# Performance work log

Measured on AMD Instinct MI355X. Metric: run time of the kernel, lower is better.

## Reference

```python
import jax, jax.numpy as jnp
import numpy as np
from jax import lax

NPOINT = 1024
RADIUS = 0.2
NSAMPLE = 32
BN_EPS = 1e-5


def square_distance(src, dst):
    # src: [B,N,3], dst: [B,M,3] -> [B,N,M]
    d = -2.0 * jnp.einsum('bnc,bmc->bnm', src, dst)
    d = d + jnp.sum(src * src, -1)[:, :, None]
    d = d + jnp.sum(dst * dst, -1)[:, None, :]
    return d


def farthest_point_sample(xyz, npoint):
    # Deterministic start at index 0 (torch version uses a random start).
    B, N, _ = xyz.shape
    batch = jnp.arange(B)

    def step(carry, _):
        distance, farthest = carry
        centroid = xyz[batch, farthest][:, None, :]          # [B,1,3]
        dist = jnp.sum((xyz - centroid) ** 2, -1)            # [B,N]
        distance = jnp.minimum(distance, dist)
        new_far = jnp.argmax(distance, -1).astype(jnp.int32)
        return (distance, new_far), farthest

    init = (jnp.full((B, N), 1e10, xyz.dtype), jnp.zeros((B,), jnp.int32))
    _, cents = lax.scan(step, init, None, length=npoint)     # [npoint,B]
    return cents.T                                           # [B,npoint]


def index_points(points, idx):
    # points: [B,N,C], idx: [B,...] -> [B,...,C]
    return jax.vmap(lambda p, i: p[i])(points, idx)


def query_ball_point(radius, nsample, xyz, new_xyz):
    B, N, _ = xyz.shape
    sqr = square_distance(new_xyz, xyz)                      # [B,S,N]
    gidx = jnp.where(sqr > radius * radius, N,
                     jnp.arange(N, dtype=jnp.int32)[None, None, :])
    gidx = jnp.sort(gidx, axis=-1)[:, :, :nsample]           # [B,S,nsample]
    first = gidx[:, :, :1]
    return jnp.where(gidx == N, first, gidx)


def conv_bn_relu(x, w, b, g, beta):
    # x: [B,Cin,K,S]; 1x1 conv + training-mode BN + ReLU
    y = jnp.einsum('bcks,oc->boks', x, w) + b[None, :, None, None]
    mean = jnp.mean(y, axis=(0, 2, 3), keepdims=True)
    var = jnp.var(y, axis=(0, 2, 3), keepdims=True)
    y = (y - mean) * lax.rsqrt(var + BN_EPS)
    y = y * g[None, :, None, None] + beta[None, :, None, None]
    return jax.nn.relu(y)


def setup_inputs() -> dict:
    key = jax.random.key(0)
    ks = jax.random.split(key, 8)
    B, N, D = 16, 4096, 64
    inp = {
        'xyz': jax.random.uniform(ks[0], (B, N, 3), jnp.float32),
        'points': jax.random.normal(ks[1], (B, N, D), jnp.float32),
        'w1': jax.random.normal(ks[2], (64, 67), jnp.float32) * 0.1,
        'b1': jax.random.normal(ks[3], (64,), jnp.float32) * 0.1,
        'g1': jnp.ones((64,), jnp.float32),
        'beta1': jnp.zeros((64,), jnp.float32),
        'w2': jax.random.normal(ks[4], (64, 64), jnp.float32) * 0.1,
        'b2': jax.random.normal(ks[5], (64,), jnp.float32) * 0.1,
        'g2': jnp.ones((64,), jnp.float32),
        'beta2': jnp.zeros((64,), jnp.float32),
        'w3': jax.random.normal(ks[6], (128, 64), jnp.float32) * 0.1,
        'b3': jax.random.normal(ks[7], (128,), jnp.float32) * 0.1,
        'g3': jnp.ones((128,), jnp.float32),
        'beta3': jnp.zeros((128,), jnp.float32),
    }
    return inp


def reference(xyz, points, w1, b1, g1, beta1, w2, b2, g2, beta2, w3, b3, g3, beta3):
    B, N, C = xyz.shape
    fps_idx = farthest_point_sample(xyz, NPOINT)                 # [B,S]
    new_xyz = index_points(xyz, fps_idx)                         # [B,S,3]
    idx = query_ball_point(RADIUS, NSAMPLE, xyz, new_xyz)        # [B,S,K]
    grouped_xyz = index_points(xyz, idx) - new_xyz[:, :, None, :]  # [B,S,K,3]
    grouped_points = jnp.concatenate([grouped_xyz, index_points(points, idx)], axis=-1)  # [B,S,K,3+D]
    x = jnp.transpose(grouped_points, (0, 3, 2, 1))              # [B,C,K,S]
    x = conv_bn_relu(x, w1, b1, g1, beta1)
    x = conv_bn_relu(x, w2, b2, g2, beta2)
    x = conv_bn_relu(x, w3, b3, g3, beta3)
    new_points = jnp.max(x, axis=2)                              # [B,C_out,S]
    new_points = jnp.transpose(new_points, (0, 2, 1))            # [B,S,C_out]
    return (new_xyz, new_points)
```

## Files before the change

kernel.cpp:

```cpp
#include <hip/hip_runtime.h>
#include <stdint.h>

#define NPOINT 1024
#define NSAMPLE 32
#define NB 16
#define NN 4096
#define BN_EPS 1e-5
#define NPIX (NB*NPOINT*NSAMPLE)
#define NBLK 8192

__device__ __forceinline__ float sqdist3(float dx, float dy, float dz) {
  #pragma clang fp contract(off)
  float a = dx*dx; float b = dy*dy; float c = dz*dz;
  return (a + b) + c;
}

#define FPS_T 512
#define FPS_PTS (NN/FPS_T)
#define FPS_W (FPS_T/64)

#define DPP_MAX64V(VAR, CTRL)                                                  \
  {                                                                            \
    long long kl = __double_as_longlong(VAR);                                  \
    int lo = (int)(unsigned int)kl, hi = (int)(kl >> 32);                      \
    int olo = __builtin_amdgcn_update_dpp(lo, lo, (CTRL), 0xf, 0xf, false);    \
    int ohi = __builtin_amdgcn_update_dpp(hi, hi, (CTRL), 0xf, 0xf, false);    \
    double ok = __longlong_as_double(((long long)ohi << 32) |                  \
                                     (unsigned long long)(unsigned int)olo);   \
    VAR = fmax(VAR, ok);                                                       \
  }

__global__ __launch_bounds__(512) void fps_kernel(
    const float* __restrict__ xyz, int* __restrict__ cents_g) {
  __shared__ __align__(16) float4 pos[NN];
  __shared__ __align__(16) double keybuf[2][FPS_W];
  __shared__ int cents_l[NPOINT];
  const int b = blockIdx.x;
  const int t = threadIdx.x;
  const float* base = xyz + (size_t)b * NN * 3;
  for (int i = t; i < NN; i += FPS_T) {
    pos[i] = make_float4(base[3*i+0], base[3*i+1], base[3*i+2], 0.f);
  }
  __syncthreads();
  float px[FPS_PTS], py[FPS_PTS], pz[FPS_PTS], dist[FPS_PTS];
  int lowj[FPS_PTS];
  #pragma unroll
  for (int i = 0; i < FPS_PTS; i++) {
    float4 p = pos[i*FPS_T + t];
    px[i] = p.x; py[i] = p.y; pz[i] = p.z;
    dist[i] = 1e10f;
    lowj[i] = (NN-1) - (i*FPS_T + t);
  }
  const int lane = t & 63, wid = t >> 6;
  int far = 0;
  for (int it = 0; it < NPOINT; it++) {
    if (t == 0) cents_l[it] = far;
    float4 c = pos[far];
    float nd[FPS_PTS];
    #pragma unroll
    for (int i = 0; i < FPS_PTS; i++) {
      float d = sqdist3(px[i]-c.x, py[i]-c.y, pz[i]-c.z);
      nd[i] = fminf(dist[i], d);
      dist[i] = nd[i];
    }
    double kk[FPS_PTS];
    #pragma unroll
    for (int i = 0; i < FPS_PTS; i++) {
      kk[i] = __longlong_as_double(
          ((long long)__float_as_int(nd[i]) << 32) |
          (unsigned long long)(unsigned int)lowj[i]);
    }
    double bk = fmax(fmax(fmax(kk[0], kk[1]), fmax(kk[2], kk[3])),
                     fmax(fmax(kk[4], kk[5]), fmax(kk[6], kk[7])));
    DPP_MAX64V(bk, 0x111);
    DPP_MAX64V(bk, 0x112);
    DPP_MAX64V(bk, 0x114);
    DPP_MAX64V(bk, 0x118);
    DPP_MAX64V(bk, 0x142);
    DPP_MAX64V(bk, 0x143);
    const int p = it & 1;
    if (lane == 63) keybuf[p][wid] = bk;
    __syncthreads();
    double k = keybuf[p][lane & (FPS_W-1)];
    DPP_MAX64V(k, 0x111);
    DPP_MAX64V(k, 0x112);
    DPP_MAX64V(k, 0x114);
    int lo32 = (int)(unsigned int)__double_as_longlong(k);
    far = (NN-1) - __builtin_amdgcn_readlane(lo32, 7);
  }
  __syncthreads();
  for (int i = t; i < NPOINT; i += FPS_T) cents_g[b*NPOINT + i] = cents_l[i];
}

__global__ __launch_bounds__(256) void ballquery_kernel(
    const float* __restrict__ xyz, const int* __restrict__ cents_g,
    int* __restrict__ idx) {
  const int w = blockIdx.x * 4 + (threadIdx.x >> 6);
  const int lane = threadIdx.x & 63;
  const int b = w >> 10;
  const double RR = 0.2 * 0.2;
  const int cj = cents_g[w] & (NN-1);
  const float* cptr = xyz + ((size_t)b * NN + cj) * 3;
  const double cx = (double)cptr[0], cy = (double)cptr[1], cz = (double)cptr[2];
  const double cn = cx*cx + cy*cy + cz*cz;
  const float* base = xyz + (size_t)b * NN * 3;
  int* out = idx + (size_t)w * NSAMPLE;
  int have = 0, firstj = 0;
  for (int j0 = 0; j0 < NN; j0 += 64) {
    int j = j0 + lane;
    double x = (double)base[3*j+0];
    double y = (double)base[3*j+1];
    double z = (double)base[3*j+2];
    double pn = x*x + y*y + z*z;
    double d = -2.0*(cx*x + cy*y + cz*z) + cn + pn;
    bool pass = !(d > RR);
    unsigned long long m = __ballot(pass);
    int cnt = __popcll(m);
    if (have == 0 && cnt > 0) firstj = j0 + (__ffsll((unsigned long long)m) - 1);
    if (pass) {
      int pos = have + __popcll(m & ((1ull << lane) - 1ull));
      if (pos < NSAMPLE) out[pos] = j;
    }
    have += cnt;
    if (have >= NSAMPLE) break;
  }
  for (int k = have + lane; k < NSAMPLE; k += 64) out[k] = firstj;
}

template<int MODE, bool STOREY>
__global__ __launch_bounds__(256) void fused_pass(
    const float* __restrict__ xyz, const float* __restrict__ points,
    const int* __restrict__ cents_g, const int* __restrict__ idx,
    const float* __restrict__ w1, const float* __restrict__ b1,
    const float* __restrict__ w2, const float* __restrict__ b2,
    const float* __restrict__ w3, const float* __restrict__ b3,
    const double* __restrict__ aff1, const double* __restrict__ aff2,
    double* __restrict__ partial, float* __restrict__ pmax, float* __restrict__ pmin,
    float* __restrict__ ystore) {
  __shared__ float wbuf[67*64];
  __shared__ float xsm[67*68];
  __shared__ float bsm[64];
  __shared__ float bsm2[64];
  __shared__ float sc1m[64], sh1m[64], sc2m[64], sh2m[64];
  const int t = threadIdx.x;
  const int pb = blockIdx.x * 64;
  const int tr = t & 15, tc = t >> 4;
  double* pout = partial + (size_t)blockIdx.x * 256;

  for (int ii = t; ii < 67*64; ii += 256) {
    int oc = ii & 63, cc = ii >> 6;
    wbuf[cc*64 + oc] = w1[oc*67 + cc];
  }
  if (t < 64) {
    bsm[t] = b1[t];
    if (MODE >= 2) { sc1m[t] = (float)aff1[t]; sh1m[t] = (float)aff1[128+t]; }
    if (MODE >= 3) { sc2m[t] = (float)aff2[t]; sh2m[t] = (float)aff2[128+t]; }
  }
  {
    const int pxl = t >> 2, q = t & 3;
    const int p = pb + pxl;
    const int bs = p >> 5;
    const int b  = p >> 15;
    const int j  = idx[p] & (NN-1);
    const float4* prow = (const float4*)(points + ((size_t)b * NN + j) * 64);
    #pragma unroll
    for (int u = 0; u < 4; u++) {
      float4 v = prow[q*4 + u];
      int c0 = 3 + q*16 + u*4;
      xsm[(c0+0)*68 + pxl] = v.x;
      xsm[(c0+1)*68 + pxl] = v.y;
      xsm[(c0+2)*68 + pxl] = v.z;
      xsm[(c0+3)*68 + pxl] = v.w;
    }
    if (q == 0) {
      const float* xr = xyz + ((size_t)b * NN + j) * 3;
      const int cj = cents_g[bs] & (NN-1);
      const float* ce = xyz + ((size_t)b * NN + cj) * 3;
      xsm[0*68 + pxl] = xr[0] - ce[0];
      xsm[1*68 + pxl] = xr[1] - ce[1];
      xsm[2*68 + pxl] = xr[2] - ce[2];
    }
  }
  __syncthreads();

  float acc[4][4] = {};
  for (int cc = 0; cc < 67; cc++) {
    float4 xv = *(const float4*)&xsm[cc*68 + 4*tr];
    float4 wv = *(const float4*)&wbuf[cc*64 + 4*tc];
    float xa[4] = {xv.x, xv.y, xv.z, xv.w};
    float wa[4] = {wv.x, wv.y, wv.z, wv.w};
    #pragma unroll
    for (int i = 0; i < 4; i++)
      #pragma unroll
      for (int jj = 0; jj < 4; jj++) acc[i][jj] += xa[i]*wa[jj];
  }
  if constexpr (MODE == 1) {
    if constexpr (STOREY) {
      #pragma unroll
      for (int i = 0; i < 4; i++) {
        float4 o = make_float4(acc[i][0], acc[i][1], acc[i][2], acc[i][3]);
        *(float4*)(ystore + ((size_t)(pb + 4*tr + i))*64 + 4*tc) = o;
      }
    }
    double s1[4] = {0,0,0,0}, s2[4] = {0,0,0,0};
    #pragma unroll
    for (int jj = 0; jj < 4; jj++) {
      float bb = bsm[4*tc+jj];
      #pragma unroll
      for (int i = 0; i < 4; i++) {
        double yd = (double)(acc[i][jj] + bb);
        s1[jj] += yd; s2[jj] += yd*yd;
      }
    }
    #pragma unroll
    for (int off = 8; off > 0; off >>= 1)
      #pragma unroll
      for (int jj = 0; jj < 4; jj++) {
        s1[jj] += __shfl_down(s1[jj], off, 16);
        s2[jj] += __shfl_down(s2[jj], off, 16);
      }
    if (tr == 0)
      #pragma unroll
      for (int jj = 0; jj < 4; jj++) {
        pout[4*tc+jj]       = s1[jj];
        pout[128 + 4*tc+jj] = s2[jj];
      }
    return;
  }

  __syncthreads();
  #pragma unroll
  for (int jj = 0; jj < 4; jj++) {
    int oc = 4*tc + jj;
    float bb = bsm[oc], sc = sc1m[oc], sh = sh1m[oc];
    float r[4];
    #pragma unroll
    for (int i = 0; i < 4; i++) r[i] = fmaxf((acc[i][jj] + bb)*sc + sh, 0.f);
    *(float4*)&xsm[oc*68 + 4*tr] = make_float4(r[0], r[1], r[2], r[3]);
  }
  for (int ii = t; ii < 4096; ii += 256) {
    int oc = ii & 63, cc = ii >> 6;
    wbuf[cc*64 + oc] = w2[oc*64 + cc];
  }
  if (t < 64) bsm2[t] = b2[t];
  __syncthreads();

  float acc2[4][4] = {};
  for (int cc = 0; cc < 64; cc++) {
    float4 xv = *(const float4*)&xsm[cc*68 + 4*tr];
    float4 wv = *(const float4*)&wbuf[cc*64 + 4*tc];
    float xa[4] = {xv.x, xv.y, xv.z, xv.w};
    float wa[4] = {wv.x, wv.y, wv.z, wv.w};
    #pragma unroll
    for (int i = 0; i < 4; i++)
      #pragma unroll
      for (int jj = 0; jj < 4; jj++) acc2[i][jj] += xa[i]*wa[jj];
  }
  if constexpr (MODE == 2) {
    if constexpr (STOREY) {
      #pragma unroll
      for (int i = 0; i < 4; i++) {
        float4 o = make_float4(acc2[i][0], acc2[i][1], acc2[i][2], acc2[i][3]);
        *(float4*)(ystore + ((size_t)(pb + 4*tr + i))*64 + 4*tc) = o;
      }
    }
    double s1[4] = {0,0,0,0}, s2[4] = {0,0,0,0};
    #pragma unroll
    for (int jj = 0; jj < 4; jj++) {
      float bb = bsm2[4*tc+jj];
      #pragma unroll
      for (int i = 0; i < 4; i++) {
        double yd = (double)(acc2[i][jj] + bb);
        s1[jj] += yd; s2[jj] += yd*yd;
      }
    }
    #pragma unroll
    for (int off = 8; off > 0; off >>= 1)
      #pragma unroll
      for (int jj = 0; jj < 4; jj++) {
        s1[jj] += __shfl_down(s1[jj], off, 16);
        s2[jj] += __shfl_down(s2[jj], off, 16);
      }
    if (tr == 0)
      #pragma unroll
      for (int jj = 0; jj < 4; jj++) {
        pout[4*tc+jj]       = s1[jj];
        pout[128 + 4*tc+jj] = s2[jj];
      }
    return;
  }

  if constexpr (MODE == 3) {
    __syncthreads();
    #pragma unroll
    for (int jj = 0; jj < 4; jj++) {
      int oc = 4*tc + jj;
      float bb = bsm2[oc], sc = sc2m[oc], sh = sh2m[oc];
      float r[4];
      #pragma unroll
      for (int i = 0; i < 4; i++) r[i] = fmaxf((acc2[i][jj] + bb)*sc + sh, 0.f);
      *(float4*)&xsm[oc*68 + 4*tr] = make_float4(r[0], r[1], r[2], r[3]);
    }
    for (int h = 0; h < 2; h++) {
      for (int ii = t; ii < 4096; ii += 256) {
        int oc = ii & 63, cc = ii >> 6;
        wbuf[cc*64 + oc] = w3[(h*64 + oc)*64 + cc];
      }
      if (t < 64) bsm[t] = b3[h*64 + t];
      __syncthreads();
      float acc3[4][4] = {};
      for (int cc = 0; cc < 64; cc++) {
        float4 xv = *(const float4*)&xsm[cc*68 + 4*tr];
        float4 wv = *(const float4*)&wbuf[cc*64 + 4*tc];
        float xa[4] = {xv.x, xv.y, xv.z, xv.w};
        float wa[4] = {wv.x, wv.y, wv.z, wv.w};
        #pragma unroll
        for (int i = 0; i < 4; i++)
          #pragma unroll
          for (int jj = 0; jj < 4; jj++) acc3[i][jj] += xa[i]*wa[jj];
      }
      double s1[4] = {0,0,0,0}, s2[4] = {0,0,0,0};
      float pmx[4], pmn[4];
      #pragma unroll
      for (int jj = 0; jj < 4; jj++) { pmx[jj] = -3.4e38f; pmn[jj] = 3.4e38f; }
      #pragma unroll
      for (int jj = 0; jj < 4; jj++) {
        float bb = bsm[4*tc+jj];
        #pragma unroll
        for (int i = 0; i < 4; i++) {
          float y = acc3[i][jj] + bb;
          double yd = (double)y;
          s1[jj] += yd; s2[jj] += yd*yd;
          pmx[jj] = fmaxf(pmx[jj], y); pmn[jj] = fminf(pmn[jj], y);
        }
      }
      #pragma unroll
      for (int off = 8; off > 0; off >>= 1)
        #pragma unroll
        for (int jj = 0; jj < 4; jj++) {
          s1[jj] += __shfl_down(s1[jj], off, 16);
          s2[jj] += __shfl_down(s2[jj], off, 16);
        }
      if (tr == 0)
        #pragma unroll
        for (int jj = 0; jj < 4; jj++) {
          pout[h*64 + 4*tc+jj]       = s1[jj];
          pout[128 + h*64 + 4*tc+jj] = s2[jj];
        }
      #pragma unroll
      for (int off = 4; off > 0; off >>= 1)
        #pragma unroll
        for (int jj = 0; jj < 4; jj++) {
          pmx[jj] = fmaxf(pmx[jj], __shfl_down(pmx[jj], off, 8));
          pmn[jj] = fminf(pmn[jj], __shfl_down(pmn[jj], off, 8));
        }
      if ((tr & 7) == 0) {
        int bs = (pb >> 5) + (tr >> 3);
        size_t ob = (size_t)bs*128 + h*64 + 4*tc;
        #pragma unroll
        for (int jj = 0; jj < 4; jj++) {
          pmax[ob + jj] = pmx[jj];
          pmin[ob + jj] = pmn[jj];
        }
      }
      __syncthreads();
    }
  }
}

__global__ __launch_bounds__(256) void fused_mid(
    const float* __restrict__ y1, const float* __restrict__ b1,
    const float* __restrict__ w2, const float* __restrict__ b2,
    const double* __restrict__ aff1,
    double* __restrict__ partial, float* __restrict__ y2) {
  __shared__ float wbuf[64*64];
  __shared__ float xsm[64*68];
  __shared__ float bsm[64];
  __shared__ float bsm2[64];
  __shared__ float sc1m[64], sh1m[64];
  const int t = threadIdx.x;
  const int pb = blockIdx.x * 64;
  const int tr = t & 15, tc = t >> 4;
  double* pout = partial + (size_t)blockIdx.x * 256;

  for (int ii = t; ii < 4096; ii += 256) {
    int oc = ii & 63, cc = ii >> 6;
    wbuf[cc*64 + oc] = w2[oc*64 + cc];
  }
  if (t < 64) {
    bsm[t] = b1[t]; bsm2[t] = b2[t];
    sc1m[t] = (float)aff1[t]; sh1m[t] = (float)aff1[128+t];
  }
  __syncthreads();
  {
    const int pxl = t >> 2, q = t & 3;
    const float* yrow = y1 + ((size_t)(pb + pxl))*64;
    #pragma unroll
    for (int u = 0; u < 4; u++) {
      int c0 = 4*q + 16*u;
      float4 v = *(const float4*)(yrow + c0);
      xsm[(c0+0)*68 + pxl] = fmaxf((v.x + bsm[c0+0])*sc1m[c0+0] + sh1m[c0+0], 0.f);
      xsm[(c0+1)*68 + pxl] = fmaxf((v.y + bsm[c0+1])*sc1m[c0+1] + sh1m[c0+1], 0.f);
      xsm[(c0+2)*68 + pxl] = fmaxf((v.z + bsm[c0+2])*sc1m[c0+2] + sh1m[c0+2], 0.f);
      xsm[(c0+3)*68 + pxl] = fmaxf((v.w + bsm[c0+3])*sc1m[c0+3] + sh1m[c0+3], 0.f);
    }
  }
  __syncthreads();

  float acc2[4][4] = {};
  for (int cc = 0; cc < 64; cc++) {
    float4 xv = *(const float4*)&xsm[cc*68 + 4*tr];
    float4 wv = *(const float4*)&wbuf[cc*64 + 4*tc];
    float xa[4] = {xv.x, xv.y, xv.z, xv.w};
    float wa[4] = {wv.x, wv.y, wv.z, wv.w};
    #pragma unroll
    for (int i = 0; i < 4; i++)
      #pragma unroll
      for (int jj = 0; jj < 4; jj++) acc2[i][jj] += xa[i]*wa[jj];
  }
  #pragma unroll
  for (int i = 0; i < 4; i++) {
    float4 o = make_float4(acc2[i][0], acc2[i][1], acc2[i][2], acc2[i][3]);
    *(float4*)(y2 + ((size_t)(pb + 4*tr + i))*64 + 4*tc) = o;
  }
  double s1[4] = {0,0,0,0}, s2[4] = {0,0,0,0};
  #pragma unroll
  for (int jj = 0; jj < 4; jj++) {
    float bb = bsm2[4*tc+jj];
    #pragma unroll
    for (int i = 0; i < 4; i++) {
      double yd = (double)(acc2[i][jj] + bb);
      s1[jj] += yd; s2[jj] += yd*yd;
    }
  }
  #pragma unroll
  for (int off = 8; off > 0; off >>= 1)
    #pragma unroll
    for (int jj = 0; jj < 4; jj++) {
      s1[jj] += __shfl_down(s1[jj], off, 16);
      s2[jj] += __shfl_down(s2[jj], off, 16);
    }
  if (tr == 0)
    #pragma unroll
    for (int jj = 0; jj < 4; jj++) {
      pout[4*tc+jj]       = s1[jj];
      pout[128 + 4*tc+jj] = s2[jj];
    }
}

__global__ __launch_bounds__(256) void fused_last(
    const float* __restrict__ y2, const float* __restrict__ b2,
    const float* __restrict__ w3, const float* __restrict__ b3,
    const double* __restrict__ aff2,
    double* __restrict__ partial, float* __restrict__ pmax, float* __restrict__ pmin) {
  __shared__ float wbuf[64*64];
  __shared__ float xsm[64*68];
  __shared__ float bsm[64];
  __shared__ float bsm2[64];
  __shared__ float sc2m[64], sh2m[64];
  const int t = threadIdx.x;
  const int pb = blockIdx.x * 64;
  const int tr = t & 15, tc = t >> 4;
  double* pout = partial + (size_t)blockIdx.x * 256;

  if (t < 64) {
    bsm2[t] = b2[t];
    sc2m[t] = (float)aff2[t]; sh2m[t] = (float)aff2[128+t];
  }
  __syncthreads();
  {
    const int pxl = t >> 2, q = t & 3;
    const float* yrow = y2 + ((size_t)(pb + pxl))*64;
    #pragma unroll
    for (int u = 0; u < 4; u++) {
      int c0 = 4*q + 16*u;
      float4 v = *(const float4*)(yrow + c0);
      xsm[(c0+0)*68 + pxl] = fmaxf((v.x + bsm2[c0+0])*sc2m[c0+0] + sh2m[c0+0], 0.f);
      xsm[(c0+1)*68 + pxl] = fmaxf((v.y + bsm2[c0+1])*sc2m[c0+1] + sh2m[c0+1], 0.f);
      xsm[(c0+2)*68 + pxl] = fmaxf((v.z + bsm2[c0+2])*sc2m[c0+2] + sh2m[c0+2], 0.f);
      xsm[(c0+3)*68 + pxl] = fmaxf((v.w + bsm2[c0+3])*sc2m[c0+3] + sh2m[c0+3], 0.f);
    }
  }
  for (int h = 0; h < 2; h++) {
    for (int ii = t; ii < 4096; ii += 256) {
      int oc = ii & 63, cc = ii >> 6;
      wbuf[cc*64 + oc] = w3[(h*64 + oc)*64 + cc];
    }
    if (t < 64) bsm[t] = b3[h*64 + t];
    __syncthreads();
    float acc3[4][4] = {};
    for (int cc = 0; cc < 64; cc++) {
      float4 xv = *(const float4*)&xsm[cc*68 + 4*tr];
      float4 wv = *(const float4*)&wbuf[cc*64 + 4*tc];
      float xa[4] = {xv.x, xv.y, xv.z, xv.w};
      float wa[4] = {wv.x, wv.y, wv.z, wv.w};
      #pragma unroll
      for (int i = 0; i < 4; i++)
        #pragma unroll
        for (int jj = 0; jj < 4; jj++) acc3[i][jj] += xa[i]*wa[jj];
    }
    double s1[4] = {0,0,0,0}, s2[4] = {0,0,0,0};
    float pmx[4], pmn[4];
    #pragma unroll
    for (int jj = 0; jj < 4; jj++) { pmx[jj] = -3.4e38f; pmn[jj] = 3.4e38f; }
    #pragma unroll
    for (int jj = 0; jj < 4; jj++) {
      float bb = bsm[4*tc+jj];
      #pragma unroll
      for (int i = 0; i < 4; i++) {
        float y = acc3[i][jj] + bb;
        double yd = (double)y;
        s1[jj] += yd; s2[jj] += yd*yd;
        pmx[jj] = fmaxf(pmx[jj], y); pmn[jj] = fminf(pmn[jj], y);
      }
    }
    #pragma unroll
    for (int off = 8; off > 0; off >>= 1)
      #pragma unroll
      for (int jj = 0; jj < 4; jj++) {
        s1[jj] += __shfl_down(s1[jj], off, 16);
        s2[jj] += __shfl_down(s2[jj], off, 16);
      }
    if (tr == 0)
      #pragma unroll
      for (int jj = 0; jj < 4; jj++) {
        pout[h*64 + 4*tc+jj]       = s1[jj];
        pout[128 + h*64 + 4*tc+jj] = s2[jj];
      }
    #pragma unroll
    for (int off = 4; off > 0; off >>= 1)
      #pragma unroll
      for (int jj = 0; jj < 4; jj++) {
        pmx[jj] = fmaxf(pmx[jj], __shfl_down(pmx[jj], off, 8));
        pmn[jj] = fminf(pmn[jj], __shfl_down(pmn[jj], off, 8));
      }
    if ((tr & 7) == 0) {
      int bs = (pb >> 5) + (tr >> 3);
      size_t ob = (size_t)bs*128 + h*64 + 4*tc;
      #pragma unroll
      for (int jj = 0; jj < 4; jj++) {
        pmax[ob + jj] = pmx[jj];
        pmin[ob + jj] = pmn[jj];
      }
    }
    __syncthreads();
  }
}

__global__ __launch_bounds__(256) void reduce_finalize_kernel(
    const double* __restrict__ partial,
    const float* __restrict__ g, const float* __restrict__ beta,
    double* __restrict__ aff) {
  __shared__ double sa1[4], sa2[4];
  const int c = blockIdx.x;
  const int t = threadIdx.x;
  double a1 = 0.0, a2 = 0.0;
  for (int blk = t; blk < NBLK; blk += 256) {
    a1 += partial[(size_t)blk*256 + c];
    a2 += partial[(size_t)blk*256 + 128 + c];
  }
  #pragma unroll
  for (int off = 32; off > 0; off >>= 1) {
    a1 += __shfl_down(a1, off);
    a2 += __shfl_down(a2, off);
  }
  const int lane = t & 63, wid = t >> 6;
  if (lane == 0) { sa1[wid] = a1; sa2[wid] = a2; }
  __syncthreads();
  if (t == 0) {
    double s1 = sa1[0] + sa1[1] + sa1[2] + sa1[3];
    double s2 = sa2[0] + sa2[1] + sa2[2] + sa2[3];
    const double invN = 1.0 / (double)NPIX;
    double mean = s1 * invN;
    double var  = s2 * invN - mean*mean;
    var = var > 0.0 ? var : 0.0;
    double r  = 1.0 / sqrt(var + BN_EPS);
    double sc = (double)g[c] * r;
    aff[c]       = sc;
    aff[128 + c] = (double)beta[c] - mean*sc;
  }
}

__global__ __launch_bounds__(256) void out_kernel(
    const float* __restrict__ pmax, const float* __restrict__ pmin,
    const double* __restrict__ aff3, float* __restrict__ out_np) {
  int i = blockIdx.x * 256 + threadIdx.x;
  int oc = i & 127;
  double sc = aff3[oc], sh = aff3[128+oc];
  double v = (sc >= 0.0) ? (double)pmax[i] : (double)pmin[i];
  double y = v*sc + sh;
  out_np[i] = (float)(y > 0.0 ? y : 0.0);
}

__global__ __launch_bounds__(1024) void write_newxyz_kernel(
    const float* __restrict__ xyz, const int* __restrict__ cents_g,
    float* __restrict__ out) {
  int i = blockIdx.x * 1024 + threadIdx.x;
  int b = i >> 10;
  int j = cents_g[i] & (NN-1);
  const float* src = xyz + ((size_t)b * NN + j) * 3;
  size_t o = (size_t)i * 3;
  out[o+0] = src[0];
  out[o+1] = src[1];
  out[o+2] = src[2];
}

extern "C" void kernel_launch(void* const* d_in, const int* in_sizes, int n_in,
                              void* d_out, int out_size, void* d_ws, size_t ws_size,
                              hipStream_t stream) {
  const float* xyz    = (const float*)d_in[0];
  const float* points = (const float*)d_in[1];
  const float* w1  = (const float*)d_in[2];
  const float* b1  = (const float*)d_in[3];
  const float* g1  = (const float*)d_in[4];
  const float* be1 = (const float*)d_in[5];
  const float* w2  = (const float*)d_in[6];
  const float* b2  = (const float*)d_in[7];
  const float* g2  = (const float*)d_in[8];
  const float* be2 = (const float*)d_in[9];
  const float* w3  = (const float*)d_in[10];
  const float* b3  = (const float*)d_in[11];
  const float* g3  = (const float*)d_in[12];
  const float* be3 = (const float*)d_in[13];

  char* ws = (char*)d_ws;
  double* aff     = (double*)(ws + 8192);
  int*    cents   = (int*)  (ws + 16384);
  int*    idx     = (int*)  (ws + 81920);
  float*  pmax    = (float*)(ws + 2179072);
  float*  pmin    = (float*)(ws + 10567680);
  double* partial = (double*)(ws + 18956288);
  const size_t OFF_Y = 35733504;
  const size_t SZ_Y  = (size_t)NPIX * 64 * 4;
  float* ycache1 = (float*)(ws + OFF_Y);
  float* ycache2 = (float*)(ws + OFF_Y + SZ_Y);
  const bool full_path = ws_size >= OFF_Y + 2*SZ_Y;
  const bool mid_path  = ws_size >= OFF_Y + SZ_Y;
  float* out_xyz = (float*)d_out;
  float* out_np  = (float*)d_out + (size_t)NB*NPOINT*3;

  fps_kernel        <<<16,   512, 0, stream>>>(xyz, cents);
  ballquery_kernel  <<<4096, 256, 0, stream>>>(xyz, cents, idx);
  if (full_path) {
    fused_pass<1,true>  <<<NBLK, 256, 0, stream>>>(xyz, points, cents, idx, w1,b1,w2,b2,w3,b3,
                                                   aff, aff+256, partial, pmax, pmin, ycache1);
    reduce_finalize_kernel<<<64, 256, 0, stream>>>(partial, g1, be1, aff);
    fused_mid         <<<NBLK, 256, 0, stream>>>(ycache1, b1, w2, b2, aff, partial, ycache2);
    reduce_finalize_kernel<<<64, 256, 0, stream>>>(partial, g2, be2, aff+256);
    fused_last        <<<NBLK, 256, 0, stream>>>(ycache2, b2, w3, b3, aff+256,
                                                 partial, pmax, pmin);
    reduce_finalize_kernel<<<128, 256, 0, stream>>>(partial, g3, be3, aff+512);
  } else if (mid_path) {
    fused_pass<1,false> <<<NBLK, 256, 0, stream>>>(xyz, points, cents, idx, w1,b1,w2,b2,w3,b3,
                                                   aff, aff+256, partial, pmax, pmin, nullptr);
    reduce_finalize_kernel<<<64, 256, 0, stream>>>(partial, g1, be1, aff);
    fused_pass<2,true>  <<<NBLK, 256, 0, stream>>>(xyz, points, cents, idx, w1,b1,w2,b2,w3,b3,
                                                   aff, aff+256, partial, pmax, pmin, ycache1);
    reduce_finalize_kernel<<<64, 256, 0, stream>>>(partial, g2, be2, aff+256);
    fused_last        <<<NBLK, 256, 0, stream>>>(ycache1, b2, w3, b3, aff+256,
                                                 partial, pmax, pmin);
    reduce_finalize_kernel<<<128, 256, 0, stream>>>(partial, g3, be3, aff+512);
  } else {
    fused_pass<1,false> <<<NBLK, 256, 0, stream>>>(xyz, points, cents, idx, w1,b1,w2,b2,w3,b3,
                                                   aff, aff+256, partial, pmax, pmin, nullptr);
    reduce_finalize_kernel<<<64, 256, 0, stream>>>(partial, g1, be1, aff);
    fused_pass<2,false> <<<NBLK, 256, 0, stream>>>(xyz, points, cents, idx, w1,b1,w2,b2,w3,b3,
                                                   aff, aff+256, partial, pmax, pmin, nullptr);
    reduce_finalize_kernel<<<64, 256, 0, stream>>>(partial, g2, be2, aff+256);
    fused_pass<3,false> <<<NBLK, 256, 0, stream>>>(xyz, points, cents, idx, w1,b1,w2,b2,w3,b3,
                                                   aff, aff+256, partial, pmax, pmin, nullptr);
    reduce_finalize_kernel<<<128, 256, 0, stream>>>(partial, g3, be3, aff+512);
  }
  out_kernel        <<<NBLK, 256, 0, stream>>>(pmax, pmin, aff+512, out_np);
  write_newxyz_kernel<<<16, 1024, 0, stream>>>(xyz, cents, out_xyz);
}
```

Measured before the change: 1.283 ms.

## Interleave two FPS batches per block and fuse new_xyz output write

The FPS kernel now runs two batches per 512-thread block, with 256 threads each. The two halves alternate phases: while one half does its cross-wave reduction to pick the next centroid, the other half computes distances and the wave-level argmax. This is meant to hide the barrier and reduction latency of the serial FPS loop, and it also cuts the cross-wave reduction to 4 waves. Gathering the sampled xyz coordinates is folded into the FPS epilogue, which removes the separate write_newxyz kernel launch. The cost is 16 points per thread instead of 8, double the shared memory, and only 8 blocks on the GPU.

Measured after the change: 1.776 ms. +38.5%, slower.

```diff
diff --git a/kernel.cpp b/kernel.cpp
--- a/kernel.cpp
+++ b/kernel.cpp
@@ -15,9 +15,9 @@
   return (a + b) + c;
 }
 
-#define FPS_T 512
+#define FPS_T 256
 #define FPS_PTS (NN/FPS_T)
-#define FPS_W (FPS_T/64)
+#define FPS_W 4
 
 #define DPP_MAX64V(VAR, CTRL)                                                  \
   {                                                                            \
@@ -30,66 +30,86 @@
     VAR = fmax(VAR, ok);                                                       \
   }
 
+#define FPS_WSTEP(K)                                                           \
+  {                                                                            \
+    if (tt == 0) cents_l[sub][(K)] = far;                                      \
+    float4 c = pos[sub][far];                                                  \
+    float nd[FPS_PTS];                                                         \
+    _Pragma("unroll")                                                          \
+    for (int i = 0; i < FPS_PTS; i++) {                                        \
+      float d = sqdist3(px[i]-c.x, py[i]-c.y, pz[i]-c.z);                      \
+      nd[i] = fminf(dist[i], d);                                               \
+      dist[i] = nd[i];                                                         \
+    }                                                                          \
+    double kk[FPS_PTS];                                                        \
+    _Pragma("unroll")                                                          \
+    for (int i = 0; i < FPS_PTS; i++)                                          \
+      kk[i] = __longlong_as_double(                                            \
+          ((long long)__float_as_int(nd[i]) << 32) |                           \
+          (unsigned long long)(unsigned int)lowj[i]);                          \
+    double m0 = fmax(fmax(kk[0],  kk[1]),  fmax(kk[2],  kk[3]));               \
+    double m1 = fmax(fmax(kk[4],  kk[5]),  fmax(kk[6],  kk[7]));               \
+    double m2 = fmax(fmax(kk[8],  kk[9]),  fmax(kk[10], kk[11]));              \
+    double m3 = fmax(fmax(kk[12], kk[13]), fmax(kk[14], kk[15]));              \
+    double bk = fmax(fmax(m0, m1), fmax(m2, m3));                              \
+    DPP_MAX64V(bk, 0x111); DPP_MAX64V(bk, 0x112); DPP_MAX64V(bk, 0x114);       \
+    DPP_MAX64V(bk, 0x118); DPP_MAX64V(bk, 0x142); DPP_MAX64V(bk, 0x143);       \
+    if (lane == 63) keybuf[sub][(K)&1][wid] = bk;                              \
+  }
+
+#define FPS_SSTEP(K)                                                           \
+  {                                                                            \
+    double k2 = keybuf[sub][(K)&1][lane & (FPS_W-1)];                          \
+    DPP_MAX64V(k2, 0x111); DPP_MAX64V(k2, 0x112);                              \
+    int lo32 = (int)(unsigned int)__double_as_longlong(k2);                    \
+    far = (NN-1) - __builtin_amdgcn_readlane(lo32, 3);                         \
+  }
+
 __global__ __launch_bounds__(512) void fps_kernel(
-    const float* __restrict__ xyz, int* __restrict__ cents_g) {
-  __shared__ __align__(16) float4 pos[NN];
-  __shared__ __align__(16) double keybuf[2][FPS_W];
-  __shared__ int cents_l[NPOINT];
-  const int b = blockIdx.x;
+    const float* __restrict__ xyz, int* __restrict__ cents_g,
+    float* __restrict__ out_xyz) {
+  __shared__ __align__(16) float4 pos[2][NN];
+  __shared__ __align__(16) double keybuf[2][2][FPS_W];
+  __shared__ int cents_l[2][NPOINT];
   const int t = threadIdx.x;
+  const int sub = t >> 8;
+  const int tt = t & 255;
+  const int b = blockIdx.x * 2 + sub;
+  const int lane = tt & 63, wid = tt >> 6;
   const float* base = xyz + (size_t)b * NN * 3;
-  for (int i = t; i < NN; i += FPS_T) {
-    pos[i] = make_float4(base[3*i+0], base[3*i+1], base[3*i+2], 0.f);
+  for (int i = tt; i < NN; i += FPS_T) {
+    pos[sub][i] = make_float4(base[3*i+0], base[3*i+1], base[3*i+2], 0.f);
   }
   __syncthreads();
   float px[FPS_PTS], py[FPS_PTS], pz[FPS_PTS], dist[FPS_PTS];
   int lowj[FPS_PTS];
   #pragma unroll
   for (int i = 0; i < FPS_PTS; i++) {
-    float4 p = pos[i*FPS_T + t];
+    float4 p = pos[sub][i*FPS_T + tt];
     px[i] = p.x; py[i] = p.y; pz[i] = p.z;
     dist[i] = 1e10f;
-    lowj[i] = (NN-1) - (i*FPS_T + t);
-  }
-  const int lane = t & 63, wid = t >> 6;
+    lowj[i] = (NN-1) - (i*FPS_T + tt);
+  }
   int far = 0;
-  for (int it = 0; it < NPOINT; it++) {
-    if (t == 0) cents_l[it] = far;
-    float4 c = pos[far];
-    float nd[FPS_PTS];
-    #pragma unroll
-    for (int i = 0; i < FPS_PTS; i++) {
-      float d = sqdist3(px[i]-c.x, py[i]-c.y, pz[i]-c.z);
-      nd[i] = fminf(dist[i], d);
-      dist[i] = nd[i];
-    }
-    double kk[FPS_PTS];
-    #pragma unroll
-    for (int i = 0; i < FPS_PTS; i++) {
-      kk[i] = __longlong_as_double(
-          ((long long)__float_as_int(nd[i]) << 32) |
-          (unsigned long long)(unsigned int)lowj[i]);
-    }
-    double bk = fmax(fmax(fmax(kk[0], kk[1]), fmax(kk[2], kk[3])),
-                     fmax(fmax(kk[4], kk[5]), fmax(kk[6], kk[7])));
-    DPP_MAX64V(bk, 0x111);
-    DPP_MAX64V(bk, 0x112);
-    DPP_MAX64V(bk, 0x114);
-    DPP_MAX64V(bk, 0x118);
-    DPP_MAX64V(bk, 0x142);
-    DPP_MAX64V(bk, 0x143);
-    const int p = it & 1;
-    if (lane == 63) keybuf[p][wid] = bk;
+  if (sub == 0) FPS_WSTEP(0);
+  __syncthreads();
+  for (int k = 0; k < NPOINT-1; k++) {
+    if (sub == 0) { FPS_SSTEP(k); } else { FPS_WSTEP(k); }
     __syncthreads();
-    double k = keybuf[p][lane & (FPS_W-1)];
-    DPP_MAX64V(k, 0x111);
-    DPP_MAX64V(k, 0x112);
-    DPP_MAX64V(k, 0x114);
-    int lo32 = (int)(unsigned int)__double_as_longlong(k);
-    far = (NN-1) - __builtin_amdgcn_readlane(lo32, 7);
-  }
-  __syncthreads();
-  for (int i = t; i < NPOINT; i += FPS_T) cents_g[b*NPOINT + i] = cents_l[i];
+    if (sub == 0) { FPS_WSTEP(k+1); } else { FPS_SSTEP(k); }
+    __syncthreads();
+  }
+  if (sub == 1) FPS_WSTEP(NPOINT-1);
+  __syncthreads();
+  for (int i = tt; i < NPOINT; i += FPS_T) {
+    int j = cents_l[sub][i];
+    cents_g[b*NPOINT + i] = j;
+    float4 p = pos[sub][j];
+    size_t o = ((size_t)b * NPOINT + i) * 3;
+    out_xyz[o+0] = p.x;
+    out_xyz[o+1] = p.y;
+    out_xyz[o+2] = p.z;
+  }
 }
 
 __global__ __launch_bounds__(256) void ballquery_kernel(
@@ -592,19 +612,6 @@
   out_np[i] = (float)(y > 0.0 ? y : 0.0);
 }
 
-__global__ __launch_bounds__(1024) void write_newxyz_kernel(
-    const float* __restrict__ xyz, const int* __restrict__ cents_g,
-    float* __restrict__ out) {
-  int i = blockIdx.x * 1024 + threadIdx.x;
-  int b = i >> 10;
-  int j = cents_g[i] & (NN-1);
-  const float* src = xyz + ((size_t)b * NN + j) * 3;
-  size_t o = (size_t)i * 3;
-  out[o+0] = src[0];
-  out[o+1] = src[1];
-  out[o+2] = src[2];
-}
-
 extern "C" void kernel_launch(void* const* d_in, const int* in_sizes, int n_in,
                               void* d_out, int out_size, void* d_ws, size_t ws_size,
                               hipStream_t stream) {
@@ -639,7 +646,7 @@
   float* out_xyz = (float*)d_out;
   float* out_np  = (float*)d_out + (size_t)NB*NPOINT*3;
 
-  fps_kernel        <<<16,   512, 0, stream>>>(xyz, cents);
+  fps_kernel        <<<8,    512, 0, stream>>>(xyz, cents, out_xyz);
   ballquery_kernel  <<<4096, 256, 0, stream>>>(xyz, cents, idx);
   if (full_path) {
     fused_pass<1,true>  <<<NBLK, 256, 0, stream>>>(xyz, points, cents, idx, w1,b1,w2,b2,w3,b3,
@@ -672,5 +679,4 @@
     reduce_finalize_kernel<<<128, 256, 0, stream>>>(partial, g3, be3, aff+512);
   }
   out_kernel        <<<NBLK, 256, 0, stream>>>(pmax, pmin, aff+512, out_np);
-  write_newxyz_kernel<<<16, 1024, 0, stream>>>(xyz, cents, out_xyz);
-}
+}
```
